# Optimization experiments

Measured on AMD Instinct MI355X. Metric: run time of the kernel, lower is better.

The kernel has to match this reference:

```python
import jax, jax.numpy as jnp
import numpy as np

EPS = 1e-5
NUM_HEADS = 32

def layer_norm(x, g, b):
    m = jnp.mean(x, axis=-1, keepdims=True)
    v = jnp.mean((x - m) ** 2, axis=-1, keepdims=True)
    return (x - m) * jax.lax.rsqrt(v + EPS) * g + b

def positional_encoding(S, E):
    pos = jnp.arange(S, dtype=jnp.float32)[:, None]
    div = jnp.exp(jnp.arange(0, E, 2, dtype=jnp.float32) * (-jnp.log(10000.0) / E))
    ang = pos * div  # [S, E/2]
    pe = jnp.zeros((S, E), jnp.float32)
    pe = pe.at[:, 0::2].set(jnp.sin(ang)).at[:, 1::2].set(jnp.cos(ang))
    return pe

def quantum_attention(x, phi_l):
    # QLayer circuit: RX(x_j + phi_j) per wire, CNOT ring, measure Z.
    # Heisenberg picture: <Z_i> = prod_{j<=i} cos(a_j) for i>=1,
    #                     <Z_0> = prod_{j>=1} cos(a_j), a_j = x_j + phi_j.
    B, S, E = x.shape
    dk = E // NUM_HEADS  # = 8 wires
    c = jnp.cos(x.reshape(B, S, NUM_HEADS, dk) + phi_l)  # per-wire <Z> factor
    pref = jnp.cumprod(c, axis=-1)                       # prod_{j<=i}
    out0 = jnp.prod(c[..., 1:], axis=-1)                 # wire 0
    q = jnp.concatenate([out0[..., None], pref[..., 1:]], axis=-1)
    q = q.reshape(B, S, E)
    scores = jax.nn.softmax(
        jnp.einsum('bse,bte->bst', q, q) / jnp.sqrt(jnp.float32(dk)), axis=-1)
    return jnp.einsum('bst,bte->bse', scores, q)

def quantum_ffn(x, theta_l, W1_l, b1_l, W2_l, b2_l):
    # QLayer: RX(x_i) then RY(theta_i) on |0>, product state => <Z_i>=cos(x_i)cos(theta_i)
    nq = theta_l.shape[0]  # 8; encoder only reads first nq features
    qm = jnp.cos(x[..., :nq]) * jnp.cos(theta_l)
    h = jax.nn.relu(qm @ W1_l + b1_l)
    return h @ W2_l + b2_l

def setup_inputs() -> dict:
    key = jax.random.key(0)
    ks = jax.random.split(key, 10)
    V, E, L, FF, NQ, NC = 32000, 256, 4, 1024, 8, 10
    B, S = 8, 2048
    return {
        'tokens': jax.random.randint(ks[0], (B, S), 0, V, dtype=jnp.int64)
            if jax.config.jax_enable_x64 else jax.random.randint(ks[0], (B, S), 0, V, dtype=jnp.int32),
        'emb': jax.random.normal(ks[1], (V, E), jnp.float32),
        'phi': jax.random.normal(ks[2], (L, NQ), jnp.float32),
        'theta': jax.random.normal(ks[3], (L, NQ), jnp.float32),
        'W1': jax.random.normal(ks[4], (L, NQ, FF), jnp.float32) * 0.1,
        'b1': jax.random.normal(ks[5], (L, FF), jnp.float32) * 0.1,
        'W2': jax.random.normal(ks[6], (L, FF, E), jnp.float32) * 0.05,
        'b2': jax.random.normal(ks[7], (L, E), jnp.float32) * 0.05,
        'g1': jnp.ones((L, E), jnp.float32),
        'beta1': jnp.zeros((L, E), jnp.float32),
        'g2': jnp.ones((L, E), jnp.float32),
        'beta2': jnp.zeros((L, E), jnp.float32),
        'Wc': jax.random.normal(ks[8], (E, NC), jnp.float32) * 0.05,
        'bc': jax.random.normal(ks[9], (NC,), jnp.float32) * 0.05,
    }

def reference(tokens, emb, phi, theta, W1, b1, W2, b2, g1, beta1, g2, beta2, Wc, bc):
    B, S = tokens.shape
    E = emb.shape[1]
    x = emb[tokens] + positional_encoding(S, E)
    for l in range(phi.shape[0]):  # fixed num_blocks loop
        a = quantum_attention(x, phi[l])
        x = layer_norm(x + a, g1[l], beta1[l])
        f = quantum_ffn(x, theta[l], W1[l], b1[l], W2[l], b2[l])
        x = layer_norm(x + f, g2[l], beta2[l])
    return jnp.mean(x, axis=1) @ Wc + bc
```

## Files before the change

kernel.cpp:

```cpp
#include <hip/hip_runtime.h>
#include <hip/hip_bf16.h>

#define B_ 8
#define S_ 2048
#define E_ 256
#define FF_ 1024
#define NQ_ 8
#define NC_ 10
#define BS_ (B_*S_)
#define NSPLIT 2
#define KVBLK 32

typedef __bf16 bf16x8 __attribute__((ext_vector_type(8)));
typedef __bf16 bf16x4 __attribute__((ext_vector_type(4)));
typedef float f32x4 __attribute__((ext_vector_type(4)));

#define MFMA16(a,b,c) __builtin_amdgcn_mfma_f32_16x16x32_bf16(a,b,c,0,0,0)

__global__ __launch_bounds__(256) void k_embqt(const int* __restrict__ tokens,
                                               const float* __restrict__ emb,
                                               const float* __restrict__ phi_l,
                                               __bf16* __restrict__ x,
                                               __bf16* __restrict__ qbf,
                                               __bf16* __restrict__ qT) {
    __shared__ __align__(16) __bf16 tile[64][76];
    int t0 = blockIdx.x * 64, e0 = blockIdx.y * 64, b = blockIdx.z;
    int tid = threadIdx.x;
    float ph[8];
#pragma unroll
    for (int j = 0; j < 8; j++) ph[j] = phi_l[j];
#pragma unroll
    for (int k = 0; k < 2; k++) {
        int idx = k * 256 + tid;
        int r = idx >> 3, hh = idx & 7;
        int s = t0 + r;
        int tok = tokens[(size_t)b * S_ + t0 + r];
        const float* ep = emb + (size_t)tok * E_ + e0 + hh * 8;
        f32x4 v0 = *(const f32x4*)ep;
        f32x4 v1 = *(const f32x4*)(ep + 4);
        float xv[8];
#pragma unroll
        for (int j = 0; j < 8; j++) {
            int e = e0 + hh * 8 + j;
            int i2 = e & ~1;
            float d = __expf((float)i2 * (-9.210340371976184f / 256.0f));
            float ang = (float)s * d;
            float pe = (e & 1) ? __cosf(ang) : __sinf(ang);
            xv[j] = ((j < 4) ? v0[j] : v1[j - 4]) + pe;
        }
        bf16x8 xb;
#pragma unroll
        for (int j = 0; j < 8; j++) xb[j] = (__bf16)xv[j];
        *(bf16x8*)(x + ((size_t)b * S_ + t0 + r) * E_ + e0 + hh * 8) = xb;
        float c[8];
#pragma unroll
        for (int j = 0; j < 8; j++) c[j] = __cosf(xv[j] + ph[j]);
        float q[8];
        float run = c[0];
#pragma unroll
        for (int i = 1; i < 8; i++) { run *= c[i]; q[i] = run; }
        float o0 = c[1];
#pragma unroll
        for (int i = 2; i < 8; i++) o0 *= c[i];
        q[0] = o0;
        bf16x8 v;
#pragma unroll
        for (int j = 0; j < 8; j++) v[j] = (__bf16)q[j];
        *(bf16x8*)(qbf + ((size_t)b * S_ + t0 + r) * E_ + e0 + hh * 8) = v;
        *(bf16x8*)&tile[r][hh * 8] = v;
    }
    __syncthreads();
#pragma unroll
    for (int k = 0; k < 2; k++) {
        int idx = k * 256 + tid;
        int el = idx >> 3, tc = idx & 7;
        bf16x8 v;
#pragma unroll
        for (int j = 0; j < 8; j++) v[j] = tile[tc * 8 + j][el];
        *(bf16x8*)(qT + ((size_t)b * E_ + e0 + el) * S_ + t0 + tc * 8) = v;
    }
}

__global__ __launch_bounds__(256, 2) void k_attn(const __hip_bfloat16* __restrict__ qbf,
                                                 const __hip_bfloat16* __restrict__ qT,
                                                 __bf16* __restrict__ pacc,
                                                 float* __restrict__ pl) {
    __shared__ __align__(16) __bf16 ktile[KVBLK * 256];
    __shared__ __align__(16) __bf16 vtile[2][256 * KVBLK];
    __shared__ __align__(16) __bf16 plds[2][32][36];
    __shared__ float redl[2][32][2];
    const float SCALE = 0.3535533905932738f;
    int bid  = blockIdx.x;
    int b    = bid & 7;
    int qt   = (bid >> 3) & 31;
    int z    = bid >> 8;
    int tid  = threadIdx.x;
    int wv   = tid >> 6;
    int lane = tid & 63;
    int r16  = lane & 15;
    int kg   = lane >> 4;
    int rg   = wv >> 1, eh = wv & 1;
    int qrow0 = qt * 64 + rg * 32;
    int ebase = eh * 128;

    bf16x8 aq[2][8];
#pragma unroll
    for (int qs = 0; qs < 2; qs++)
#pragma unroll
        for (int kk = 0; kk < 8; kk++)
            aq[qs][kk] = *(const bf16x8*)(qbf + ((size_t)b * S_ + qrow0 + qs * 16 + r16) * E_ + kk * 32 + kg * 8);

    f32x4 acc0[8], acc1[8];
#pragma unroll
    for (int cf = 0; cf < 8; cf++) { acc0[cf] = (f32x4){0.f,0.f,0.f,0.f}; acc1[cf] = (f32x4){0.f,0.f,0.f,0.f}; }
    float lrow0[4] = {0.f,0.f,0.f,0.f}, lrow1[4] = {0.f,0.f,0.f,0.f};

    constexpr int SPAN = S_ / NSPLIT;
    constexpr int NT = SPAN / KVBLK;
    int k0 = z * SPAN;

    auto issue_k = [&](int kb) {
#pragma unroll
        for (int c = 0; c < 4; c++) {
            int seg = wv * 4 + c;
            int r = seg * 2 + (lane >> 5);
            int ch = lane & 31;
            const __hip_bfloat16* src = qbf + ((size_t)b * S_ + kb + r) * E_ + ((ch ^ (r & 7)) * 8);
            __builtin_amdgcn_global_load_lds((const __attribute__((address_space(1))) void*)src,
                                             (__attribute__((address_space(3))) void*)(ktile + seg * 512),
                                             16, 0, 0);
        }
    };
    auto issue_v = [&](int kb, int buf) {
#pragma unroll
        for (int c = 0; c < 4; c++) {
            int seg = wv * 4 + c;
            int e = seg * 16 + (lane >> 2);
            int ch = lane & 3;
            const __hip_bfloat16* src = qT + ((size_t)b * E_ + e) * S_ + kb + ((ch ^ ((e >> 1) & 3)) * 8);
            __builtin_amdgcn_global_load_lds((const __attribute__((address_space(1))) void*)src,
                                             (__attribute__((address_space(3))) void*)(&vtile[buf][seg * 512]),
                                             16, 0, 0);
        }
    };

    issue_k(k0);
    issue_v(k0, 0);
    asm volatile("s_waitcnt vmcnt(0)" ::: "memory");
    __syncthreads();

    for (int kt = 0; kt < NT; kt++) {
        int vcur = kt & 1;
        f32x4 s0 = (f32x4){0.f,0.f,0.f,0.f}, s1 = (f32x4){0.f,0.f,0.f,0.f};
#pragma unroll
        for (int kk = 0; kk < 8; kk++) {
            bf16x8 bk = *(const bf16x8*)&ktile[(eh * 16 + r16) * 256 + (((kk * 4 + kg) ^ (r16 & 7)) * 8)];
            s0 = MFMA16(aq[0][kk], bk, s0);
            s1 = MFMA16(aq[1][kk], bk, s1);
        }
#pragma unroll
        for (int i = 0; i < 4; i++) {
            float p0 = __expf(fmaf(s0[i], SCALE, -44.0f));
            float p1 = __expf(fmaf(s1[i], SCALE, -44.0f));
            plds[rg][kg * 4 + i][eh * 16 + r16]      = (__bf16)p0;
            plds[rg][16 + kg * 4 + i][eh * 16 + r16] = (__bf16)p1;
            lrow0[i] += p0;
            lrow1[i] += p1;
        }
        __syncthreads();
        bool more = (kt + 1 < NT);
        if (more) {
            int kn = k0 + (kt + 1) * KVBLK;
            issue_k(kn);
            issue_v(kn, vcur ^ 1);
        }
        bf16x8 pa0 = *(const bf16x8*)&plds[rg][r16][kg * 8];
        bf16x8 pa1 = *(const bf16x8*)&plds[rg][16 + r16][kg * 8];
#pragma unroll
        for (int cf = 0; cf < 8; cf++) {
            int vrow = ebase + cf * 16 + r16;
            bf16x8 bv = *(const bf16x8*)&vtile[vcur][vrow * KVBLK + ((kg ^ ((vrow >> 1) & 3)) * 8)];
            acc0[cf] = MFMA16(pa0, bv, acc0[cf]);
            acc1[cf] = MFMA16(pa1, bv, acc1[cf]);
        }
        if (more) {
            asm volatile("s_waitcnt vmcnt(0)" ::: "memory");
            __syncthreads();
        }
    }

#pragma unroll
    for (int i = 0; i < 4; i++) {
#pragma unroll
        for (int m = 1; m <= 8; m <<= 1) {
            lrow0[i] += __shfl_xor(lrow0[i], m);
            lrow1[i] += __shfl_xor(lrow1[i], m);
        }
    }
    if (r16 == 0) {
#pragma unroll
        for (int i = 0; i < 4; i++) {
            redl[rg][kg * 4 + i][eh]      = lrow0[i];
            redl[rg][16 + kg * 4 + i][eh] = lrow1[i];
        }
    }
    __syncthreads();
    size_t prow0 = (size_t)z * BS_ + (size_t)b * S_ + qrow0;
    if (eh == 0 && r16 == 0) {
#pragma unroll
        for (int i = 0; i < 4; i++) {
            int q = kg * 4 + i;
            pl[prow0 + q]      = redl[rg][q][0] + redl[rg][q][1];
            pl[prow0 + 16 + q] = redl[rg][16 + q][0] + redl[rg][16 + q][1];
        }
    }
#pragma unroll
    for (int i = 0; i < 4; i++) {
#pragma unroll
        for (int cf = 0; cf < 8; cf++) {
            pacc[(prow0 + kg * 4 + i) * E_ + ebase + cf * 16 + r16]      = (__bf16)acc0[cf][i];
            pacc[(prow0 + 16 + kg * 4 + i) * E_ + ebase + cf * 16 + r16] = (__bf16)acc1[cf][i];
        }
    }
}

__global__ __launch_bounds__(256) void k_aln(const __bf16* __restrict__ pacc,
                                             const float* __restrict__ pl,
                                             __bf16* __restrict__ x,
                                             const float* __restrict__ g,
                                             const float* __restrict__ bb) {
    int wv = threadIdx.x >> 6, lane = threadIdx.x & 63;
    size_t row = (size_t)blockIdx.x * 4 + wv;
    float inv = 1.0f / (pl[row] + pl[BS_ + row]);
    bf16x4 a0 = ((const bf16x4*)(pacc + row * E_))[lane];
    bf16x4 a1 = ((const bf16x4*)(pacc + (size_t)BS_ * E_ + row * E_))[lane];
    bf16x4 xv = ((const bf16x4*)(x + row * E_))[lane];
    f32x4 v;
    float s = 0.f, sq = 0.f;
#pragma unroll
    for (int j = 0; j < 4; j++) {
        v[j] = (float)xv[j] + ((float)a0[j] + (float)a1[j]) * inv;
        s += v[j]; sq += v[j] * v[j];
    }
#pragma unroll
    for (int m = 1; m <= 32; m <<= 1) { s += __shfl_xor(s, m); sq += __shfl_xor(sq, m); }
    float mean = s * (1.f / E_);
    float var = sq * (1.f / E_) - mean * mean;
    float rstd = rsqrtf(var + 1e-5f);
    f32x4 gv = ((const f32x4*)g)[lane];
    f32x4 bv = ((const f32x4*)bb)[lane];
    bf16x4 o;
#pragma unroll
    for (int j = 0; j < 4; j++) o[j] = (__bf16)((v[j] - mean) * rstd * gv[j] + bv[j]);
    ((bf16x4*)(x + row * E_))[lane] = o;
}

__global__ __launch_bounds__(256) void k_w2t(const float* __restrict__ W2,
                                             __hip_bfloat16* __restrict__ w2t) {
    __shared__ __align__(16) __bf16 tile[64][72];
    int k0 = blockIdx.x * 64, e0 = blockIdx.y * 64, l = blockIdx.z;
    const float* W2l = W2 + (size_t)l * FF_ * E_;
    __hip_bfloat16* w2tl = w2t + (size_t)l * E_ * FF_;
    int tid = threadIdx.x;
#pragma unroll
    for (int half = 0; half < 2; half++) {
        int r  = half * 32 + (tid >> 3);
        int c8 = (tid & 7) * 8;
        f32x4 v0 = *(const f32x4*)(W2l + (size_t)(k0 + r) * E_ + e0 + c8);
        f32x4 v1 = *(const f32x4*)(W2l + (size_t)(k0 + r) * E_ + e0 + c8 + 4);
#pragma unroll
        for (int j = 0; j < 4; j++) { tile[r][c8 + j] = (__bf16)v0[j]; tile[r][c8 + 4 + j] = (__bf16)v1[j]; }
    }
    __syncthreads();
#pragma unroll
    for (int half = 0; half < 2; half++) {
        int e  = half * 32 + (tid >> 3);
        int k8 = (tid & 7) * 8;
        bf16x8 v;
#pragma unroll
        for (int j = 0; j < 8; j++) v[j] = tile[k8 + j][e];
        *(bf16x8*)(w2tl + (size_t)(e0 + e) * FF_ + k0 + k8) = v;
    }
}

__global__ __launch_bounds__(256) void k_ffn(__bf16* __restrict__ x,
                                             const float* __restrict__ theta_l,
                                             const float* __restrict__ W1l,
                                             const float* __restrict__ b1l,
                                             const __hip_bfloat16* __restrict__ w2t,
                                             const float* __restrict__ b2l,
                                             const float* __restrict__ g,
                                             const float* __restrict__ bb,
                                             const float* __restrict__ phi_next,
                                             __bf16* __restrict__ qbf,
                                             __bf16* __restrict__ qT,
                                             float* __restrict__ psum,
                                             int gen_q) {
    __shared__ __align__(16) __bf16 Bld[2][256 * 64];
    __shared__ __align__(16) __bf16 Ald[2][32 * 64];
    __shared__ float qmld[32][9];
    __shared__ float reds[32][4][2];
    int tid = threadIdx.x;
    int wv = tid >> 6, lane = tid & 63;
    int r16 = lane & 15, kg = lane >> 4;
    int rbase = blockIdx.x * 32;
    int ebQ = wv * 64;
    const int NT = FF_ / 64;

    {
        int r = tid >> 3, i = tid & 7;
        qmld[r][i] = __cosf((float)x[(size_t)(rbase + r) * E_ + i]) * __cosf(theta_l[i]);
    }

    f32x4 w[18];

    auto issue_B = [&](int kt, int buf) {
#pragma unroll
        for (int s = 0; s < 8; s++) {
            int seg = wv * 8 + s;
            int e = seg * 8 + (lane >> 3);
            int c = lane & 7;
            const __hip_bfloat16* src = w2t + (size_t)e * FF_ + kt * 64 + ((c ^ (e & 7)) * 8);
            __builtin_amdgcn_global_load_lds((const __attribute__((address_space(1))) void*)src,
                                             (__attribute__((address_space(3))) void*)(&Bld[buf][seg * 512]),
                                             16, 0, 0);
        }
    };
    auto load_W1 = [&](int kt) {
        int c = tid & 7;
        int k = kt * 64 + c * 8;
#pragma unroll
        for (int i = 0; i < 8; i++) {
            w[2 * i]     = *(const f32x4*)(W1l + (size_t)i * FF_ + k);
            w[2 * i + 1] = *(const f32x4*)(W1l + (size_t)i * FF_ + k + 4);
        }
        w[16] = *(const f32x4*)(b1l + k);
        w[17] = *(const f32x4*)(b1l + k + 4);
    };
    auto math_h = [&](int buf) {
        int r = tid >> 3, c = tid & 7;
        f32x4 h0 = w[16], h1 = w[17];
#pragma unroll
        for (int i = 0; i < 8; i++) {
            float qv = qmld[r][i];
#pragma unroll
            for (int j = 0; j < 4; j++) {
                h0[j] = fmaf(qv, w[2 * i][j], h0[j]);
                h1[j] = fmaf(qv, w[2 * i + 1][j], h1[j]);
            }
        }
        bf16x8 hv;
#pragma unroll
        for (int j = 0; j < 4; j++) {
            hv[j]     = (__bf16)fmaxf(h0[j], 0.f);
            hv[4 + j] = (__bf16)fmaxf(h1[j], 0.f);
        }
        *(bf16x8*)&Ald[buf][r * 64 + ((c ^ (r & 7)) * 8)] = hv;
    };

    issue_B(0, 0);
    load_W1(0);
    __syncthreads();
    math_h(0);
    __syncthreads();

    f32x4 acc[2][4];
#pragma unroll
    for (int qs = 0; qs < 2; qs++)
#pragma unroll
        for (int cf = 0; cf < 4; cf++) acc[qs][cf] = (f32x4){0.f, 0.f, 0.f, 0.f};

    for (int kt = 0; kt < NT; kt++) {
        int cur = kt & 1;
        bool more = (kt + 1 < NT);
        if (more) {
            issue_B(kt + 1, cur ^ 1);
            load_W1(kt + 1);
        }
        bf16x8 aq[2][2];
#pragma unroll
        for (int qs = 0; qs < 2; qs++)
#pragma unroll
            for (int kk = 0; kk < 2; kk++)
                aq[qs][kk] = *(const bf16x8*)&Ald[cur][(qs * 16 + r16) * 64 + (((kk * 4 + kg) ^ (r16 & 7)) * 8)];
#pragma unroll
        for (int cf = 0; cf < 4; cf++) {
            int e = ebQ + cf * 16 + r16;
#pragma unroll
            for (int kk = 0; kk < 2; kk++) {
                bf16x8 bv = *(const bf16x8*)&Bld[cur][e * 64 + (((kk * 4 + kg) ^ (e & 7)) * 8)];
                acc[0][cf] = MFMA16(aq[0][kk], bv, acc[0][cf]);
                acc[1][cf] = MFMA16(aq[1][kk], bv, acc[1][cf]);
            }
        }
        if (more) {
            math_h(cur ^ 1);
            __syncthreads();
        }
    }

    float sA[2][4] = {{0.f,0.f,0.f,0.f},{0.f,0.f,0.f,0.f}};
    float sQ[2][4] = {{0.f,0.f,0.f,0.f},{0.f,0.f,0.f,0.f}};
#pragma unroll
    for (int qs = 0; qs < 2; qs++)
#pragma unroll
        for (int cf = 0; cf < 4; cf++) {
            int e = ebQ + cf * 16 + r16;
            float b2v = b2l[e];
#pragma unroll
            for (int i = 0; i < 4; i++) {
                size_t orow = (size_t)rbase + qs * 16 + kg * 4 + i;
                float t = acc[qs][cf][i] + b2v + (float)x[orow * E_ + e];
                acc[qs][cf][i] = t;
                sA[qs][i] += t; sQ[qs][i] += t * t;
            }
        }
#pragma unroll
    for (int qs = 0; qs < 2; qs++)
#pragma unroll
        for (int i = 0; i < 4; i++) {
#pragma unroll
            for (int m = 1; m <= 8; m <<= 1) {
                sA[qs][i] += __shfl_xor(sA[qs][i], m);
                sQ[qs][i] += __shfl_xor(sQ[qs][i], m);
            }
        }
    if (r16 == 0) {
#pragma unroll
        for (int qs = 0; qs < 2; qs++)
#pragma unroll
            for (int i = 0; i < 4; i++) {
                int row = qs * 16 + kg * 4 + i;
                reds[row][wv][0] = sA[qs][i];
                reds[row][wv][1] = sQ[qs][i];
            }
    }
    __syncthreads();
    float mean[2][4], rstd[2][4];
#pragma unroll
    for (int qs = 0; qs < 2; qs++)
#pragma unroll
        for (int i = 0; i < 4; i++) {
            int row = qs * 16 + kg * 4 + i;
            float S = reds[row][0][0] + reds[row][1][0] + reds[row][2][0] + reds[row][3][0];
            float Q = reds[row][0][1] + reds[row][1][1] + reds[row][2][1] + reds[row][3][1];
            mean[qs][i] = S * (1.f / E_);
            float var = Q * (1.f / E_) - mean[qs][i] * mean[qs][i];
            rstd[qs][i] = rsqrtf(var + 1e-5f);
        }
#pragma unroll
    for (int qs = 0; qs < 2; qs++)
#pragma unroll
        for (int cf = 0; cf < 4; cf++) {
            int e = ebQ + cf * 16 + r16;
            float gv = g[e], bv = bb[e];
#pragma unroll
            for (int i = 0; i < 4; i++) {
                size_t orow = (size_t)rbase + qs * 16 + kg * 4 + i;
                float xn = (acc[qs][cf][i] - mean[qs][i]) * rstd[qs][i] * gv + bv;
                acc[qs][cf][i] = xn;
                if (gen_q) x[orow * E_ + e] = (__bf16)xn;
            }
        }
    if (gen_q) {
        int bq = rbase / S_;
        int trow0 = rbase % S_;
        float ph = phi_next[r16 & 7];
        int hp = r16 & 7;
#pragma unroll
        for (int qs = 0; qs < 2; qs++)
#pragma unroll
            for (int cf = 0; cf < 4; cf++) {
                int e = ebQ + cf * 16 + r16;
#pragma unroll
                for (int i = 0; i < 4; i++) {
                    float c = __cosf(acc[qs][cf][i] + ph);
                    float scan = c;
                    float cp = (hp == 0) ? 1.f : c;
#pragma unroll
                    for (int d = 1; d <= 4; d <<= 1) {
                        float t1 = __shfl_up(scan, d, 8);
                        float t2 = __shfl_up(cp, d, 8);
                        if (hp >= d) { scan *= t1; cp *= t2; }
                    }
                    float q0 = __shfl(cp, 7, 8);
                    float qv = (hp == 0) ? q0 : scan;
                    int trow = trow0 + qs * 16 + kg * 4 + i;
                    __bf16 qb = (__bf16)qv;
                    qbf[((size_t)bq * S_ + trow) * E_ + e] = qb;
                    qT[((size_t)bq * E_ + e) * S_ + trow]  = qb;
                }
            }
    } else {
#pragma unroll
        for (int cf = 0; cf < 4; cf++) {
            int e = ebQ + cf * 16 + r16;
            float s = 0.f;
#pragma unroll
            for (int qs = 0; qs < 2; qs++)
#pragma unroll
                for (int i = 0; i < 4; i++) s += acc[qs][cf][i];
            s += __shfl_xor(s, 16);
            s += __shfl_xor(s, 32);
            if (kg == 0) psum[(size_t)blockIdx.x * E_ + e] = s;
        }
    }
}

__global__ __launch_bounds__(256) void k_mean2(const float* __restrict__ psum, float* __restrict__ xmean) {
    int b = blockIdx.x, e = threadIdx.x;
    float s = 0.f;
    for (int c = 0; c < 64; c++) s += psum[((size_t)(b * 64 + c)) * E_ + e];
    xmean[b * E_ + e] = s * (1.f / S_);
}

__global__ __launch_bounds__(128) void k_cls(const float* __restrict__ xmean,
                                             const float* __restrict__ Wc,
                                             const float* __restrict__ bc,
                                             float* __restrict__ outp) {
    int t = threadIdx.x;
    if (t >= B_ * NC_) return;
    int b = t / NC_, c = t % NC_;
    float s = bc[c];
    for (int e = 0; e < E_; e++) s += xmean[b * E_ + e] * Wc[e * NC_ + c];
    outp[t] = s;
}

extern "C" void kernel_launch(void* const* d_in, const int* in_sizes, int n_in,
                              void* d_out, int out_size, void* d_ws, size_t ws_size,
                              hipStream_t stream) {
    (void)in_sizes; (void)n_in; (void)out_size; (void)ws_size;
    const int*   tokens = (const int*)d_in[0];
    const float* emb    = (const float*)d_in[1];
    const float* phi    = (const float*)d_in[2];
    const float* theta  = (const float*)d_in[3];
    const float* W1     = (const float*)d_in[4];
    const float* b1     = (const float*)d_in[5];
    const float* W2     = (const float*)d_in[6];
    const float* b2     = (const float*)d_in[7];
    const float* g1     = (const float*)d_in[8];
    const float* beta1  = (const float*)d_in[9];
    const float* g2     = (const float*)d_in[10];
    const float* beta2  = (const float*)d_in[11];
    const float* Wc     = (const float*)d_in[12];
    const float* bc     = (const float*)d_in[13];
    float* outp = (float*)d_out;

    __bf16* xbuf = (__bf16*)d_ws;
    __hip_bfloat16* qbf = (__hip_bfloat16*)(xbuf + (size_t)BS_ * E_);
    __hip_bfloat16* qT  = qbf + (size_t)BS_ * E_;
    __hip_bfloat16* w2t = qT + (size_t)BS_ * E_;
    float* psum  = (float*)(w2t + (size_t)4 * E_ * FF_);
    float* xmean = psum + (size_t)512 * E_;
    float* pl    = xmean + B_ * E_;
    __bf16* pacc = (__bf16*)(pl + (size_t)NSPLIT * BS_);

    k_w2t<<<dim3(FF_ / 64, E_ / 64, 4), 256, 0, stream>>>(W2, w2t);
    k_embqt<<<dim3(S_ / 64, E_ / 64, B_), 256, 0, stream>>>(tokens, emb, phi,
                                                            xbuf, (__bf16*)qbf, (__bf16*)qT);

    for (int l = 0; l < 4; l++) {
        k_attn<<<(S_ / 64) * B_ * NSPLIT, 256, 0, stream>>>(qbf, qT, pacc, pl);
        k_aln<<<BS_ / 4, 256, 0, stream>>>(pacc, pl, xbuf, g1 + l * E_, beta1 + l * E_);
        int gen_q = (l < 3) ? 1 : 0;
        const float* phn = phi + (size_t)(gen_q ? (l + 1) : 0) * NQ_;
        k_ffn<<<BS_ / 32, 256, 0, stream>>>(xbuf, theta + l * NQ_,
                                            W1 + (size_t)l * NQ_ * FF_, b1 + (size_t)l * FF_,
                                            w2t + (size_t)l * E_ * FF_, b2 + (size_t)l * E_,
                                            g2 + l * E_, beta2 + l * E_,
                                            phn, (__bf16*)qbf, (__bf16*)qT, psum, gen_q);
    }

    k_mean2<<<8, 256, 0, stream>>>(psum, xmean);
    k_cls<<<1, 128, 0, stream>>>(xmean, Wc, bc, outp);
}
```

Baseline: 402.0 us.

## Fuse attention split-reduce and layernorm into attention kernel via last-block counter

Removes the separate k_aln launch per layer. Each attention block increments a per-tile atomic counter, and whichever of the two KV-split blocks finishes second combines both partial accumulators, applies the residual and layernorm, and writes x. This saves a kernel launch and lets the combine overlap with other attention blocks. In exchange it adds threadfence and atomic overhead, a serial tail in the last block, and a memset of the counters.

```diff
diff --git a/kernel.cpp b/kernel.cpp
--- a/kernel.cpp
+++ b/kernel.cpp
@@ -84,11 +84,16 @@
 __global__ __launch_bounds__(256, 2) void k_attn(const __hip_bfloat16* __restrict__ qbf,
                                                  const __hip_bfloat16* __restrict__ qT,
                                                  __bf16* __restrict__ pacc,
-                                                 float* __restrict__ pl) {
+                                                 float* __restrict__ pl,
+                                                 __bf16* __restrict__ x,
+                                                 const float* __restrict__ g,
+                                                 const float* __restrict__ bb,
+                                                 int* __restrict__ ctr) {
     __shared__ __align__(16) __bf16 ktile[KVBLK * 256];
     __shared__ __align__(16) __bf16 vtile[2][256 * KVBLK];
     __shared__ __align__(16) __bf16 plds[2][32][36];
     __shared__ float redl[2][32][2];
+    __shared__ int is_last;
     const float SCALE = 0.3535533905932738f;
     int bid  = blockIdx.x;
     int b    = bid & 7;
@@ -222,37 +227,40 @@
             pacc[(prow0 + 16 + kg * 4 + i) * E_ + ebase + cf * 16 + r16] = (__bf16)acc1[cf][i];
         }
     }
-}
-
-__global__ __launch_bounds__(256) void k_aln(const __bf16* __restrict__ pacc,
-                                             const float* __restrict__ pl,
-                                             __bf16* __restrict__ x,
-                                             const float* __restrict__ g,
-                                             const float* __restrict__ bb) {
-    int wv = threadIdx.x >> 6, lane = threadIdx.x & 63;
-    size_t row = (size_t)blockIdx.x * 4 + wv;
-    float inv = 1.0f / (pl[row] + pl[BS_ + row]);
-    bf16x4 a0 = ((const bf16x4*)(pacc + row * E_))[lane];
-    bf16x4 a1 = ((const bf16x4*)(pacc + (size_t)BS_ * E_ + row * E_))[lane];
-    bf16x4 xv = ((const bf16x4*)(x + row * E_))[lane];
-    f32x4 v;
-    float s = 0.f, sq = 0.f;
-#pragma unroll
-    for (int j = 0; j < 4; j++) {
-        v[j] = (float)xv[j] + ((float)a0[j] + (float)a1[j]) * inv;
-        s += v[j]; sq += v[j] * v[j];
-    }
-#pragma unroll
-    for (int m = 1; m <= 32; m <<= 1) { s += __shfl_xor(s, m); sq += __shfl_xor(sq, m); }
-    float mean = s * (1.f / E_);
-    float var = sq * (1.f / E_) - mean * mean;
-    float rstd = rsqrtf(var + 1e-5f);
-    f32x4 gv = ((const f32x4*)g)[lane];
-    f32x4 bv = ((const f32x4*)bb)[lane];
-    bf16x4 o;
-#pragma unroll
-    for (int j = 0; j < 4; j++) o[j] = (__bf16)((v[j] - mean) * rstd * gv[j] + bv[j]);
-    ((bf16x4*)(x + row * E_))[lane] = o;
+
+    __threadfence();
+    __syncthreads();
+    if (tid == 0) is_last = (atomicAdd(&ctr[bid & 255], 1) == 1);
+    __syncthreads();
+    if (is_last) {
+        int rowbase = qt * 64;
+#pragma unroll 1
+        for (int it = 0; it < 16; it++) {
+            size_t row = (size_t)b * S_ + rowbase + it * 4 + wv;
+            float inv = 1.0f / (pl[row] + pl[BS_ + row]);
+            bf16x4 a0 = ((const bf16x4*)(pacc + row * E_))[lane];
+            bf16x4 a1 = ((const bf16x4*)(pacc + (size_t)BS_ * E_ + row * E_))[lane];
+            bf16x4 xv4 = ((const bf16x4*)(x + row * E_))[lane];
+            f32x4 v;
+            float s = 0.f, sq = 0.f;
+#pragma unroll
+            for (int j = 0; j < 4; j++) {
+                v[j] = (float)xv4[j] + ((float)a0[j] + (float)a1[j]) * inv;
+                s += v[j]; sq += v[j] * v[j];
+            }
+#pragma unroll
+            for (int m = 1; m <= 32; m <<= 1) { s += __shfl_xor(s, m); sq += __shfl_xor(sq, m); }
+            float mean = s * (1.f / E_);
+            float var = sq * (1.f / E_) - mean * mean;
+            float rstd = rsqrtf(var + 1e-5f);
+            f32x4 gv = ((const f32x4*)g)[lane];
+            f32x4 bv = ((const f32x4*)bb)[lane];
+            bf16x4 o;
+#pragma unroll
+            for (int j = 0; j < 4; j++) o[j] = (__bf16)((v[j] - mean) * rstd * gv[j] + bv[j]);
+            ((bf16x4*)(x + row * E_))[lane] = o;
+        }
+    }
 }
 
 __global__ __launch_bounds__(256) void k_w2t(const float* __restrict__ W2,
@@ -554,14 +562,17 @@
     float* xmean = psum + (size_t)512 * E_;
     float* pl    = xmean + B_ * E_;
     __bf16* pacc = (__bf16*)(pl + (size_t)NSPLIT * BS_);
-
+    int* ctr     = (int*)(pacc + (size_t)NSPLIT * BS_ * E_);
+
+    hipMemsetAsync(ctr, 0, 4 * 256 * sizeof(int), stream);
     k_w2t<<<dim3(FF_ / 64, E_ / 64, 4), 256, 0, stream>>>(W2, w2t);
     k_embqt<<<dim3(S_ / 64, E_ / 64, B_), 256, 0, stream>>>(tokens, emb, phi,
                                                             xbuf, (__bf16*)qbf, (__bf16*)qT);
 
     for (int l = 0; l < 4; l++) {
-        k_attn<<<(S_ / 64) * B_ * NSPLIT, 256, 0, stream>>>(qbf, qT, pacc, pl);
-        k_aln<<<BS_ / 4, 256, 0, stream>>>(pacc, pl, xbuf, g1 + l * E_, beta1 + l * E_);
+        k_attn<<<(S_ / 64) * B_ * NSPLIT, 256, 0, stream>>>(qbf, qT, pacc, pl,
+                                                            xbuf, g1 + l * E_, beta1 + l * E_,
+                                                            ctr + l * 256);
         int gen_q = (l < 3) ? 1 : 0;
         const float* phn = phi + (size_t)(gen_q ? (l + 1) : 0) * NQ_;
         k_ffn<<<BS_ / 32, 256, 0, stream>>>(xbuf, theta + l * NQ_,
```

Result: slower. 697.7 us (+73.5%).
